# Kernel tuning notes

Measured on AMD Instinct MI355X. Metric: run time of the kernel, lower is better.

The kernel has to match this reference:

```python
import jax, jax.numpy as jnp
import numpy as np

N, F_IN, HID, C, E = 100000, 1024, 16, 64, 3200000
BN_EPS = 1e-5


def setup_inputs() -> dict:
    key = jax.random.key(0)
    ks = jax.random.split(key, 8)
    x = jax.random.normal(ks[0], (N, F_IN), jnp.float32)
    edge_index = jax.random.randint(ks[1], (2, E), 0, N, dtype=jnp.int32)
    w1 = jax.random.normal(ks[2], (F_IN, HID), jnp.float32) / np.float32(np.sqrt(F_IN))
    b1 = jnp.zeros((HID,), jnp.float32)
    w2 = jax.random.normal(ks[3], (HID, C), jnp.float32) / np.float32(np.sqrt(HID))
    b2 = jnp.zeros((C,), jnp.float32)
    mlp_w = jax.random.normal(ks[4], (C, C), jnp.float32) / np.float32(np.sqrt(C))
    mlp_b = jnp.zeros((C,), jnp.float32)
    bn_gamma = jnp.ones((C,), jnp.float32)
    bn_beta = jnp.zeros((C,), jnp.float32)
    # per-node channel weight param, xavier_normal_ init on shape (N, 1)
    xavier_std = np.float32(np.sqrt(2.0 / (N + 1)))
    weight_raw = jax.random.normal(ks[5], (N, 1), jnp.float32) * xavier_std
    return {"x": x, "edge_index": edge_index, "w1": w1, "b1": b1, "w2": w2,
            "b2": b2, "mlp_w": mlp_w, "mlp_b": mlp_b, "bn_gamma": bn_gamma,
            "bn_beta": bn_beta, "weight_raw": weight_raw}


def _gcn_norm(edge_index, n):
    # PyG GCNConv default: add self-loops, norm = deg^-1/2[src] * deg^-1/2[dst]
    loop = jnp.arange(n, dtype=edge_index.dtype)
    src = jnp.concatenate([edge_index[0], loop])
    dst = jnp.concatenate([edge_index[1], loop])
    deg = jax.ops.segment_sum(jnp.ones_like(dst, dtype=jnp.float32), dst, num_segments=n)
    dis = jax.lax.rsqrt(jnp.maximum(deg, 1.0))  # deg >= 1 with self-loops
    norm = dis[src] * dis[dst]
    return src, dst, norm


def _gcn_conv(h, src, dst, norm, w, b, n):
    h = h @ w                              # [N, out] dense transform first
    msg = h[src] * norm[:, None]           # gather + scale per edge
    out = jax.ops.segment_sum(msg, dst, num_segments=n)  # scatter-add
    return out + b


def reference(x, edge_index, w1, b1, w2, b2, mlp_w, mlp_b, bn_gamma, bn_beta, weight_raw):
    n = x.shape[0]
    src, dst, norm = _gcn_norm(edge_index, n)
    h = _gcn_conv(x, src, dst, norm, w1, b1, n)
    h = jax.nn.relu(h)                     # dropout is identity in eval mode
    h = _gcn_conv(h, src, dst, norm, w2, b2, n)
    h = jax.nn.log_softmax(h, axis=1)
    h = jnp.exp(weight_raw) * h            # exp(xavier param) channel weight
    h = h @ mlp_w + mlp_b                  # final MLP (C*1 -> C)
    mean = jnp.mean(h, axis=0)
    var = jnp.mean(jnp.square(h - mean), axis=0)  # biased var, BN training stats
    h = (h - mean) * jax.lax.rsqrt(var + BN_EPS) * bn_gamma + bn_beta
    return jax.nn.log_softmax(h, axis=1)
```

## Files before the change

kernel.cpp:

```cpp
#include <hip/hip_runtime.h>
#include <math.h>

#define NN   100000
#define FIN  1024
#define HIDN 16
#define CCH  64
#define EE   3200000
#define BNEPS 1e-5f
#define NB   ((NN + 255) / 256)
#define NPART 8
#define PSZ  (NN / NPART)

typedef __attribute__((ext_vector_type(8))) short bf16x8;
typedef __attribute__((ext_vector_type(4))) float f32x4;

__global__ __launch_bounds__(256) void k_hist(const int* __restrict__ ei,
                                              unsigned* __restrict__ deg) {
  int p = blockIdx.x & 7;
  int blk = blockIdx.x >> 3;
  int nblk = gridDim.x >> 3;
  int lo = p * PSZ, hi = lo + PSZ;
  for (int e = blk * 256 + threadIdx.x; e < EE; e += nblk * 256) {
    int d = ei[EE + e];
    if (d >= lo && d < hi) atomicAdd(&deg[d], 1u);
  }
}

__global__ __launch_bounds__(256) void k_scan_part(const unsigned* __restrict__ deg,
                                                   unsigned* __restrict__ exc,
                                                   unsigned* __restrict__ bsum) {
  __shared__ unsigned s[256];
  int t = threadIdx.x, i = blockIdx.x * 256 + t;
  unsigned v = (i < NN) ? deg[i] : 0u;
  s[t] = v;
  __syncthreads();
#pragma unroll
  for (int off = 1; off < 256; off <<= 1) {
    unsigned u = (t >= off) ? s[t - off] : 0u;
    __syncthreads();
    s[t] += u;
    __syncthreads();
  }
  if (i < NN) exc[i] = s[t] - v;
  if (t == 255) bsum[blockIdx.x] = s[255];
}

__global__ __launch_bounds__(512) void k_scan_boff(const unsigned* __restrict__ bsum,
                                                   unsigned* __restrict__ boff) {
  __shared__ unsigned s[512];
  int t = threadIdx.x;
  unsigned v = (t < NB) ? bsum[t] : 0u;
  s[t] = v;
  __syncthreads();
#pragma unroll
  for (int off = 1; off < 512; off <<= 1) {
    unsigned u = (t >= off) ? s[t - off] : 0u;
    __syncthreads();
    s[t] += u;
    __syncthreads();
  }
  if (t < NB) boff[t] = s[t] - v;
}

__global__ __launch_bounds__(256) void k_scan_final(const unsigned* __restrict__ exc,
                                                    const unsigned* __restrict__ boff,
                                                    const unsigned* __restrict__ deg,
                                                    int* __restrict__ rowptr,
                                                    int* __restrict__ cur,
                                                    float* __restrict__ dis) {
  int i = blockIdx.x * 256 + threadIdx.x;
  if (i < NN) {
    int r = (int)(boff[i >> 8] + exc[i]);
    rowptr[i] = r;
    cur[i] = r;
    dis[i] = rsqrtf((float)(deg[i] + 1u));
  } else if (i == NN) {
    rowptr[NN] = EE;
  }
}

__global__ __launch_bounds__(256) void k_place(const int* __restrict__ ei,
                                               int* __restrict__ cur,
                                               int* __restrict__ perm) {
  int p = blockIdx.x & 7;
  int blk = blockIdx.x >> 3;
  int nblk = gridDim.x >> 3;
  int lo = p * PSZ, hi = lo + PSZ;
  for (int e = blk * 256 + threadIdx.x; e < EE; e += nblk * 256) {
    int d = ei[EE + e];
    if (d >= lo && d < hi) {
      int s = ei[e];
      int slot = atomicAdd(&cur[d], 1);
      perm[slot] = s;
    }
  }
}

__device__ __forceinline__ unsigned pk_bf16(float lo, float hi) {
  unsigned ul = __float_as_uint(lo);
  unsigned uh = __float_as_uint(hi);
  ul = (ul + 0x7fffu + ((ul >> 16) & 1u)) >> 16;
  uh = (uh + 0x7fffu + ((uh >> 16) & 1u)) & 0xffff0000u;
  return ul | uh;
}

__global__ __launch_bounds__(256, 4) void k_gemm1(const float* __restrict__ x,
                                                  const float* __restrict__ w1,
                                                  const float* __restrict__ dis,
                                                  float* __restrict__ xw1s) {
  __shared__ __align__(16) unsigned short w1t[16 * 1032];
  for (int idx = threadIdx.x; idx < 1024 * 16; idx += 256) {
    int k = idx >> 4, j = idx & 15;
    unsigned u = __float_as_uint(w1[idx]);
    u = (u + 0x7fffu + ((u >> 16) & 1u)) >> 16;
    w1t[j * 1032 + k] = (unsigned short)u;
  }
  __syncthreads();

  const int lane = threadIdx.x & 63;
  const int wave = threadIdx.x >> 6;
  const int m = lane & 15;
  const int kg = lane >> 4;

  const unsigned short* bbase = &w1t[m * 1032 + kg * 8];

#pragma unroll
  for (int t = 0; t < 4; ++t) {
    int row0 = blockIdx.x * 256 + wave * 64 + t * 16;
    int rowA = min(row0 + m, NN - 1);
    const float* xrow = x + (size_t)rowA * FIN + kg * 8;

    f32x4 acc = {0.0f, 0.0f, 0.0f, 0.0f};

#pragma unroll
    for (int ks = 0; ks < 32; ks += 4) {
      f32x4 A0[4], A1[4];
#pragma unroll
      for (int u = 0; u < 4; ++u) {
        const f32x4* pa = (const f32x4*)(xrow + (ks + u) * 32);
        A0[u] = __builtin_nontemporal_load(pa);
        A1[u] = __builtin_nontemporal_load(pa + 1);
      }
#pragma unroll
      for (int u = 0; u < 4; ++u) {
        union { unsigned w[4]; bf16x8 s; } af;
        af.w[0] = pk_bf16(A0[u].x, A0[u].y);
        af.w[1] = pk_bf16(A0[u].z, A0[u].w);
        af.w[2] = pk_bf16(A1[u].x, A1[u].y);
        af.w[3] = pk_bf16(A1[u].z, A1[u].w);
        bf16x8 bfrag = *(const bf16x8*)(bbase + (ks + u) * 32);
        acc = __builtin_amdgcn_mfma_f32_16x16x32_bf16(af.s, bfrag, acc, 0, 0, 0);
      }
    }

#pragma unroll
    for (int r = 0; r < 4; ++r) {
      int grow = row0 + kg * 4 + r;
      if (grow < NN) xw1s[grow * HIDN + m] = acc[r] * dis[grow];
    }
  }
}

__global__ __launch_bounds__(256) void k_agg1(const int* __restrict__ rowptr,
                                              const int* __restrict__ perm,
                                              const float* __restrict__ dis,
                                              const float* __restrict__ sfs,
                                              const float* __restrict__ b1,
                                              float* __restrict__ out) {
  int g = blockIdx.x * 4 + (threadIdx.x >> 6);
  if (g >= NN) return;
  int lane = threadIdx.x & 63;
  int eo = lane >> 4;
  int j = lane & 15;
  int beg = rowptr[g], end = rowptr[g + 1];
  float acc0 = 0.0f, acc1 = 0.0f;
  int e = beg + eo;
  for (; e + 4 < end; e += 8) {
    int s0 = perm[e];
    int s1 = perm[e + 4];
    acc0 += sfs[(size_t)s0 * HIDN + j];
    acc1 += sfs[(size_t)s1 * HIDN + j];
  }
  if (e < end) acc0 += sfs[(size_t)perm[e] * HIDN + j];
  float acc = acc0 + acc1;
  acc += __shfl_xor(acc, 16, 64);
  acc += __shfl_xor(acc, 32, 64);
  if (eo == 0) {
    float di = dis[g];
    float v = di * (acc + sfs[(size_t)g * HIDN + j]);
    out[(size_t)g * HIDN + j] = fmaxf(v + b1[j], 0.0f) * di;
  }
}

__global__ __launch_bounds__(256) void k_aggfuse(const int* __restrict__ rowptr,
                                                 const int* __restrict__ perm,
                                                 const float* __restrict__ dis,
                                                 const float* __restrict__ sfs,
                                                 const float* __restrict__ w2,
                                                 const float* __restrict__ b2,
                                                 const float* __restrict__ mlpw,
                                                 const float* __restrict__ mlpb,
                                                 const float* __restrict__ wraw,
                                                 float* __restrict__ out) {
  __shared__ __align__(16) float2 w2p[8 * CCH];
  __shared__ __align__(16) float2 mlpp[32 * CCH];
  __shared__ __align__(16) float avbuf[4][HIDN];
  __shared__ __align__(16) float gbuf[4][CCH];
  for (int idx = threadIdx.x; idx < 8 * CCH; idx += 256) {
    int k2 = idx >> 6, j = idx & 63;
    w2p[idx] = make_float2(w2[(2 * k2) * CCH + j], w2[(2 * k2 + 1) * CCH + j]);
  }
  for (int idx = threadIdx.x; idx < 32 * CCH; idx += 256) {
    int c2 = idx >> 6, j = idx & 63;
    mlpp[idx] = make_float2(mlpw[(2 * c2) * CCH + j], mlpw[(2 * c2 + 1) * CCH + j]);
  }
  __syncthreads();

  const int g = blockIdx.x * 4 + (threadIdx.x >> 6);
  if (g >= NN) return;
  const int lane = threadIdx.x & 63;
  const int wave = threadIdx.x >> 6;
  const int eo = lane >> 4;
  const int jc = lane & 15;
  const int j = lane;

  int beg = rowptr[g], end = rowptr[g + 1];
  float acc0 = 0.0f, acc1 = 0.0f;
  int e = beg + eo;
  for (; e + 4 < end; e += 8) {
    int s0 = perm[e];
    int s1 = perm[e + 4];
    acc0 += sfs[(size_t)s0 * HIDN + jc];
    acc1 += sfs[(size_t)s1 * HIDN + jc];
  }
  if (e < end) acc0 += sfs[(size_t)perm[e] * HIDN + jc];
  float acc = acc0 + acc1;
  acc += __shfl_xor(acc, 16, 64);
  acc += __shfl_xor(acc, 32, 64);
  float di = dis[g];
  float av = di * (acc + sfs[(size_t)g * HIDN + jc]);
  if (lane < HIDN) avbuf[wave][lane] = av;

  float2 h2p = make_float2(0.0f, 0.0f);
#pragma unroll
  for (int k2 = 0; k2 < 8; ++k2) {
    float2 a = *(const float2*)&avbuf[wave][2 * k2];
    float2 wv = w2p[k2 * CCH + j];
    h2p.x = fmaf(a.x, wv.x, h2p.x);
    h2p.y = fmaf(a.y, wv.y, h2p.y);
  }
  float h2 = h2p.x + h2p.y + b2[j];

  float mx = h2;
#pragma unroll
  for (int o = 32; o >= 1; o >>= 1) mx = fmaxf(mx, __shfl_xor(mx, o, 64));
  float ex = __expf(h2 - mx);
  float se = ex;
#pragma unroll
  for (int o = 32; o >= 1; o >>= 1) se += __shfl_xor(se, o, 64);
  float lsm = h2 - mx - __logf(se);

  float gg = __expf(wraw[g]) * lsm;
  gbuf[wave][j] = gg;

  float2 mp = make_float2(0.0f, 0.0f);
#pragma unroll
  for (int c2 = 0; c2 < 32; ++c2) {
    float2 gv = *(const float2*)&gbuf[wave][2 * c2];
    float2 wv = mlpp[c2 * CCH + j];
    mp.x = fmaf(gv.x, wv.x, mp.x);
    mp.y = fmaf(gv.y, wv.y, mp.y);
  }
  out[(size_t)g * CCH + j] = mp.x + mp.y + mlpb[j];
}

__global__ __launch_bounds__(256) void k_bnstats(const float* __restrict__ out,
                                                 double* __restrict__ gsum,
                                                 double* __restrict__ gsq) {
  __shared__ double reds[256];
  __shared__ double redq[256];
  const int lane = threadIdx.x & 63;
  const int wave = threadIdx.x >> 6;
  double s = 0.0, q = 0.0;
  for (int i = blockIdx.x * 4 + wave; i < NN; i += gridDim.x * 4) {
    float m = out[(size_t)i * CCH + lane];
    s += (double)m;
    q = fma((double)m, (double)m, q);
  }
  reds[threadIdx.x] = s;
  redq[threadIdx.x] = q;
  __syncthreads();
  if (threadIdx.x < 64) {
    double ss = reds[threadIdx.x] + reds[threadIdx.x + 64] +
                reds[threadIdx.x + 128] + reds[threadIdx.x + 192];
    double qq = redq[threadIdx.x] + redq[threadIdx.x + 64] +
                redq[threadIdx.x + 128] + redq[threadIdx.x + 192];
    atomicAdd(&gsum[threadIdx.x], ss);
    atomicAdd(&gsq[threadIdx.x], qq);
  }
}

__global__ void k_stats(const double* __restrict__ gsum,
                        const double* __restrict__ gsq,
                        const float* __restrict__ gamma,
                        const float* __restrict__ beta,
                        float* __restrict__ bnp) {
  int j = threadIdx.x;
  if (j >= CCH) return;
  const double inv_n = 1.0 / (double)NN;
  double mean = gsum[j] * inv_n;
  double var = gsq[j] * inv_n - mean * mean;
  float sc = (float)(rsqrt(var + (double)BNEPS)) * gamma[j];
  bnp[j] = (float)mean;
  bnp[CCH + j] = sc;
  bnp[2 * CCH + j] = beta[j];
}

__global__ __launch_bounds__(256) void k_out(float* __restrict__ out,
                                             const float* __restrict__ bnp) {
  const int lane = threadIdx.x & 63;
  const int wave = threadIdx.x >> 6;
  const int j = lane;
  const float mean = bnp[j];
  const float sc = bnp[CCH + j];
  const float bt = bnp[2 * CCH + j];
  const int gw = blockIdx.x * 4 + wave;
  const int nw = gridDim.x * 4;
  for (int i = gw; i < NN; i += nw) {
    float m = out[(size_t)i * CCH + j];
    float y = fmaf(m - mean, sc, bt);
    float mx = y;
#pragma unroll
    for (int o = 32; o >= 1; o >>= 1) mx = fmaxf(mx, __shfl_xor(mx, o, 64));
    float ex = __expf(y - mx);
    float se = ex;
#pragma unroll
    for (int o = 32; o >= 1; o >>= 1) se += __shfl_xor(se, o, 64);
    out[(size_t)i * CCH + j] = y - mx - __logf(se);
  }
}

extern "C" void kernel_launch(void* const* d_in, const int* in_sizes, int n_in,
                              void* d_out, int out_size, void* d_ws, size_t ws_size,
                              hipStream_t stream) {
  const float* x     = (const float*)d_in[0];
  const int*   ei    = (const int*)d_in[1];
  const float* w1    = (const float*)d_in[2];
  const float* b1    = (const float*)d_in[3];
  const float* w2    = (const float*)d_in[4];
  const float* b2    = (const float*)d_in[5];
  const float* mlpw  = (const float*)d_in[6];
  const float* mlpb  = (const float*)d_in[7];
  const float* gamma = (const float*)d_in[8];
  const float* beta  = (const float*)d_in[9];
  const float* wraw  = (const float*)d_in[10];
  float* out = (float*)d_out;

  char* w = (char*)d_ws;
  size_t off = 0;
  auto take = [&](size_t bytes) -> void* {
    void* p = w + off;
    off = (off + bytes + 255) & ~(size_t)255;
    return p;
  };
  unsigned* deg    = (unsigned*)take((size_t)NN * 4);
  float*    dis    = (float*)take((size_t)NN * 4);
  unsigned* exc    = (unsigned*)take((size_t)NN * 4);
  unsigned* bsum   = (unsigned*)take((size_t)NB * 4);
  unsigned* boff   = (unsigned*)take((size_t)NB * 4);
  int*      rowptr = (int*)take((size_t)(NN + 1) * 4);
  int*      cur    = (int*)take((size_t)NN * 4);
  int*      perm   = (int*)take((size_t)EE * 4);
  float*    xw1s   = (float*)take((size_t)NN * HIDN * 4);
  float*    rh1s   = (float*)take((size_t)NN * HIDN * 4);
  double*   gsum   = (double*)take(CCH * 8);
  double*   gsq    = (double*)take(CCH * 8);
  float*    bnp    = (float*)take(3 * CCH * 4);
  (void)ws_size; (void)n_in; (void)in_sizes; (void)out_size;

  hipMemsetAsync(deg, 0, (size_t)NN * 4, stream);
  hipMemsetAsync(gsum, 0, CCH * 8, stream);
  hipMemsetAsync(gsq, 0, CCH * 8, stream);

  k_hist<<<2048, 256, 0, stream>>>(ei, deg);
  k_scan_part<<<NB, 256, 0, stream>>>(deg, exc, bsum);
  k_scan_boff<<<1, 512, 0, stream>>>(bsum, boff);
  k_scan_final<<<(NN + 256) / 256 + 1, 256, 0, stream>>>(exc, boff, deg, rowptr, cur, dis);
  k_place<<<2048, 256, 0, stream>>>(ei, cur, perm);

  k_gemm1<<<(NN + 255) / 256, 256, 0, stream>>>(x, w1, dis, xw1s);
  k_agg1<<<(NN + 3) / 4, 256, 0, stream>>>(rowptr, perm, dis, xw1s, b1, rh1s);
  k_aggfuse<<<(NN + 3) / 4, 256, 0, stream>>>(rowptr, perm, dis, rh1s, w2, b2,
                                              mlpw, mlpb, wraw, out);

  k_bnstats<<<256, 256, 0, stream>>>(out, gsum, gsq);
  k_stats<<<1, 64, 0, stream>>>(gsum, gsq, gamma, beta, bnp);
  k_out<<<1024, 256, 0, stream>>>(out, bnp);
}
```

Baseline: 613.5 us.

## Vectorize edge loads, pre-convert W1 to bf16, shrink GEMM tile, fold BN stats

```diff
diff --git a/kernel.cpp b/kernel.cpp
--- a/kernel.cpp
+++ b/kernel.cpp
@@ -20,9 +20,12 @@
   int blk = blockIdx.x >> 3;
   int nblk = gridDim.x >> 3;
   int lo = p * PSZ, hi = lo + PSZ;
-  for (int e = blk * 256 + threadIdx.x; e < EE; e += nblk * 256) {
-    int d = ei[EE + e];
-    if (d >= lo && d < hi) atomicAdd(&deg[d], 1u);
+  for (int e4 = (blk * 256 + threadIdx.x) * 4; e4 < EE; e4 += nblk * 256 * 4) {
+    int4 d4 = *(const int4*)(ei + EE + e4);
+    if (d4.x >= lo && d4.x < hi) atomicAdd(&deg[d4.x], 1u);
+    if (d4.y >= lo && d4.y < hi) atomicAdd(&deg[d4.y], 1u);
+    if (d4.z >= lo && d4.z < hi) atomicAdd(&deg[d4.z], 1u);
+    if (d4.w >= lo && d4.w < hi) atomicAdd(&deg[d4.w], 1u);
   }
 }
 
@@ -86,13 +89,12 @@
   int blk = blockIdx.x >> 3;
   int nblk = gridDim.x >> 3;
   int lo = p * PSZ, hi = lo + PSZ;
-  for (int e = blk * 256 + threadIdx.x; e < EE; e += nblk * 256) {
-    int d = ei[EE + e];
-    if (d >= lo && d < hi) {
-      int s = ei[e];
-      int slot = atomicAdd(&cur[d], 1);
-      perm[slot] = s;
-    }
+  for (int e4 = (blk * 256 + threadIdx.x) * 4; e4 < EE; e4 += nblk * 256 * 4) {
+    int4 d4 = *(const int4*)(ei + EE + e4);
+    if (d4.x >= lo && d4.x < hi) perm[atomicAdd(&cur[d4.x], 1)] = ei[e4 + 0];
+    if (d4.y >= lo && d4.y < hi) perm[atomicAdd(&cur[d4.y], 1)] = ei[e4 + 1];
+    if (d4.z >= lo && d4.z < hi) perm[atomicAdd(&cur[d4.z], 1)] = ei[e4 + 2];
+    if (d4.w >= lo && d4.w < hi) perm[atomicAdd(&cur[d4.w], 1)] = ei[e4 + 3];
   }
 }
 
@@ -104,60 +106,58 @@
   return ul | uh;
 }
 
-__global__ __launch_bounds__(256, 4) void k_gemm1(const float* __restrict__ x,
-                                                  const float* __restrict__ w1,
-                                                  const float* __restrict__ dis,
-                                                  float* __restrict__ xw1s) {
-  __shared__ __align__(16) unsigned short w1t[16 * 1032];
-  for (int idx = threadIdx.x; idx < 1024 * 16; idx += 256) {
+__global__ __launch_bounds__(256) void k_w1bf16(const float* __restrict__ w1,
+                                                unsigned short* __restrict__ w1b) {
+  for (int idx = blockIdx.x * 256 + threadIdx.x; idx < 1024 * 16;
+       idx += gridDim.x * 256) {
     int k = idx >> 4, j = idx & 15;
     unsigned u = __float_as_uint(w1[idx]);
     u = (u + 0x7fffu + ((u >> 16) & 1u)) >> 16;
-    w1t[j * 1032 + k] = (unsigned short)u;
-  }
-  __syncthreads();
-
+    w1b[j * 1024 + k] = (unsigned short)u;
+  }
+}
+
+__global__ __launch_bounds__(256) void k_gemm1(const float* __restrict__ x,
+                                               const unsigned short* __restrict__ w1b,
+                                               const float* __restrict__ dis,
+                                               float* __restrict__ xw1s) {
   const int lane = threadIdx.x & 63;
   const int wave = threadIdx.x >> 6;
   const int m = lane & 15;
   const int kg = lane >> 4;
 
-  const unsigned short* bbase = &w1t[m * 1032 + kg * 8];
-
-#pragma unroll
-  for (int t = 0; t < 4; ++t) {
-    int row0 = blockIdx.x * 256 + wave * 64 + t * 16;
-    int rowA = min(row0 + m, NN - 1);
-    const float* xrow = x + (size_t)rowA * FIN + kg * 8;
-
-    f32x4 acc = {0.0f, 0.0f, 0.0f, 0.0f};
-
-#pragma unroll
-    for (int ks = 0; ks < 32; ks += 4) {
-      f32x4 A0[4], A1[4];
-#pragma unroll
-      for (int u = 0; u < 4; ++u) {
-        const f32x4* pa = (const f32x4*)(xrow + (ks + u) * 32);
-        A0[u] = __builtin_nontemporal_load(pa);
-        A1[u] = __builtin_nontemporal_load(pa + 1);
-      }
-#pragma unroll
-      for (int u = 0; u < 4; ++u) {
-        union { unsigned w[4]; bf16x8 s; } af;
-        af.w[0] = pk_bf16(A0[u].x, A0[u].y);
-        af.w[1] = pk_bf16(A0[u].z, A0[u].w);
-        af.w[2] = pk_bf16(A1[u].x, A1[u].y);
-        af.w[3] = pk_bf16(A1[u].z, A1[u].w);
-        bf16x8 bfrag = *(const bf16x8*)(bbase + (ks + u) * 32);
-        acc = __builtin_amdgcn_mfma_f32_16x16x32_bf16(af.s, bfrag, acc, 0, 0, 0);
-      }
+  int row0 = blockIdx.x * 64 + wave * 16;
+  int rowA = min(row0 + m, NN - 1);
+  const float* xrow = x + (size_t)rowA * FIN + kg * 8;
+  const unsigned short* bbase = w1b + m * 1024 + kg * 8;
+
+  f32x4 acc = {0.0f, 0.0f, 0.0f, 0.0f};
+
+#pragma unroll
+  for (int ks = 0; ks < 32; ks += 4) {
+    f32x4 A0[4], A1[4];
+#pragma unroll
+    for (int u = 0; u < 4; ++u) {
+      const f32x4* pa = (const f32x4*)(xrow + (ks + u) * 32);
+      A0[u] = __builtin_nontemporal_load(pa);
+      A1[u] = __builtin_nontemporal_load(pa + 1);
     }
-
-#pragma unroll
-    for (int r = 0; r < 4; ++r) {
-      int grow = row0 + kg * 4 + r;
-      if (grow < NN) xw1s[grow * HIDN + m] = acc[r] * dis[grow];
+#pragma unroll
+    for (int u = 0; u < 4; ++u) {
+      union { unsigned w[4]; bf16x8 s; } af;
+      af.w[0] = pk_bf16(A0[u].x, A0[u].y);
+      af.w[1] = pk_bf16(A0[u].z, A0[u].w);
+      af.w[2] = pk_bf16(A1[u].x, A1[u].y);
+      af.w[3] = pk_bf16(A1[u].z, A1[u].w);
+      bf16x8 bfrag = *(const bf16x8*)(bbase + (ks + u) * 32);
+      acc = __builtin_amdgcn_mfma_f32_16x16x32_bf16(af.s, bfrag, acc, 0, 0, 0);
     }
+  }
+
+#pragma unroll
+  for (int r = 0; r < 4; ++r) {
+    int grow = row0 + kg * 4 + r;
+    if (grow < NN) xw1s[grow * HIDN + m] = acc[r] * dis[grow];
   }
 }
 
@@ -300,30 +300,20 @@
   }
 }
 
-__global__ void k_stats(const double* __restrict__ gsum,
-                        const double* __restrict__ gsq,
-                        const float* __restrict__ gamma,
-                        const float* __restrict__ beta,
-                        float* __restrict__ bnp) {
-  int j = threadIdx.x;
-  if (j >= CCH) return;
-  const double inv_n = 1.0 / (double)NN;
-  double mean = gsum[j] * inv_n;
-  double var = gsq[j] * inv_n - mean * mean;
-  float sc = (float)(rsqrt(var + (double)BNEPS)) * gamma[j];
-  bnp[j] = (float)mean;
-  bnp[CCH + j] = sc;
-  bnp[2 * CCH + j] = beta[j];
-}
-
 __global__ __launch_bounds__(256) void k_out(float* __restrict__ out,
-                                             const float* __restrict__ bnp) {
+                                             const double* __restrict__ gsum,
+                                             const double* __restrict__ gsq,
+                                             const float* __restrict__ gamma,
+                                             const float* __restrict__ beta) {
   const int lane = threadIdx.x & 63;
   const int wave = threadIdx.x >> 6;
   const int j = lane;
-  const float mean = bnp[j];
-  const float sc = bnp[CCH + j];
-  const float bt = bnp[2 * CCH + j];
+  const double inv_n = 1.0 / (double)NN;
+  double md = gsum[j] * inv_n;
+  double var = gsq[j] * inv_n - md * md;
+  const float sc = (float)(rsqrt(var + (double)BNEPS)) * gamma[j];
+  const float mean = (float)md;
+  const float bt = beta[j];
   const int gw = blockIdx.x * 4 + wave;
   const int nw = gridDim.x * 4;
   for (int i = gw; i < NN; i += nw) {
@@ -363,19 +353,19 @@
     off = (off + bytes + 255) & ~(size_t)255;
     return p;
   };
-  unsigned* deg    = (unsigned*)take((size_t)NN * 4);
-  float*    dis    = (float*)take((size_t)NN * 4);
-  unsigned* exc    = (unsigned*)take((size_t)NN * 4);
-  unsigned* bsum   = (unsigned*)take((size_t)NB * 4);
-  unsigned* boff   = (unsigned*)take((size_t)NB * 4);
-  int*      rowptr = (int*)take((size_t)(NN + 1) * 4);
-  int*      cur    = (int*)take((size_t)NN * 4);
-  int*      perm   = (int*)take((size_t)EE * 4);
-  float*    xw1s   = (float*)take((size_t)NN * HIDN * 4);
-  float*    rh1s   = (float*)take((size_t)NN * HIDN * 4);
-  double*   gsum   = (double*)take(CCH * 8);
-  double*   gsq    = (double*)take(CCH * 8);
-  float*    bnp    = (float*)take(3 * CCH * 4);
+  unsigned*       deg    = (unsigned*)take((size_t)NN * 4);
+  float*          dis    = (float*)take((size_t)NN * 4);
+  unsigned*       exc    = (unsigned*)take((size_t)NN * 4);
+  unsigned*       bsum   = (unsigned*)take((size_t)NB * 4);
+  unsigned*       boff   = (unsigned*)take((size_t)NB * 4);
+  int*            rowptr = (int*)take((size_t)(NN + 1) * 4);
+  int*            cur    = (int*)take((size_t)NN * 4);
+  int*            perm   = (int*)take((size_t)EE * 4);
+  float*          xw1s   = (float*)take((size_t)NN * HIDN * 4);
+  float*          rh1s   = (float*)take((size_t)NN * HIDN * 4);
+  unsigned short* w1b    = (unsigned short*)take((size_t)16 * 1024 * 2);
+  double*         gsum   = (double*)take(CCH * 8);
+  double*         gsq    = (double*)take(CCH * 8);
   (void)ws_size; (void)n_in; (void)in_sizes; (void)out_size;
 
   hipMemsetAsync(deg, 0, (size_t)NN * 4, stream);
@@ -388,12 +378,12 @@
   k_scan_final<<<(NN + 256) / 256 + 1, 256, 0, stream>>>(exc, boff, deg, rowptr, cur, dis);
   k_place<<<2048, 256, 0, stream>>>(ei, cur, perm);
 
-  k_gemm1<<<(NN + 255) / 256, 256, 0, stream>>>(x, w1, dis, xw1s);
+  k_w1bf16<<<16, 256, 0, stream>>>(w1, w1b);
+  k_gemm1<<<(NN + 63) / 64, 256, 0, stream>>>(x, w1b, dis, xw1s);
   k_agg1<<<(NN + 3) / 4, 256, 0, stream>>>(rowptr, perm, dis, xw1s, b1, rh1s);
   k_aggfuse<<<(NN + 3) / 4, 256, 0, stream>>>(rowptr, perm, dis, rh1s, w2, b2,
                                               mlpw, mlpb, wraw, out);
 
   k_bnstats<<<256, 256, 0, stream>>>(out, gsum, gsq);
-  k_stats<<<1, 64, 0, stream>>>(gsum, gsq, gamma, beta, bnp);
-  k_out<<<1024, 256, 0, stream>>>(out, bnp);
-}
+  k_out<<<1024, 256, 0, stream>>>(out, gsum, gsq, gamma, beta);
+}
```

After: 633.0 us. +3.2%, slower.
